# Performance work log

Hardware: AMD Instinct MI355X
Metric: run time of the kernel (lower is better)

Reference implementation:

```python
import jax, jax.numpy as jnp
import numpy as np
from jax import lax

B, T, V, LAT, U, P = 256, 128, 42, 200, 512, 3  # batch, seq, vocab, latent, lstm units, num_prop


def setup_inputs() -> dict:
    key = jax.random.key(0)
    ks = jax.random.split(key, 40)
    g = lambda i, shape, s=0.05: (jax.random.normal(ks[i], shape, jnp.float32) * s)
    inp = {
        'X': jax.random.randint(ks[0], (B, T), 0, V, jnp.int64 if jax.config.jax_enable_x64 else jnp.int32),
        'Y': jax.random.randint(ks[1], (B, T), 0, V, jnp.int32),
        'C': jax.random.normal(ks[2], (B, P), jnp.float32),
        'L': jax.random.randint(ks[3], (B,), 1, T + 1, jnp.int32),
        'eps': jax.random.normal(ks[4], (B, LAT), jnp.float32),
        'emb_enc': g(5, (V, LAT), 0.1),
        'emb_dec': g(6, (V, LAT), 0.1),
        # encoder stacked LSTM: layer0 input dim = LAT + P, layers 1-2 input dim = U
        'enc_k0': g(7, (LAT + P, 4 * U)), 'enc_rk0': g(8, (U, 4 * U)), 'enc_b0': jnp.zeros((4 * U,), jnp.float32),
        'enc_k1': g(9, (U, 4 * U)), 'enc_rk1': g(10, (U, 4 * U)), 'enc_b1': jnp.zeros((4 * U,), jnp.float32),
        'enc_k2': g(11, (U, 4 * U)), 'enc_rk2': g(12, (U, 4 * U)), 'enc_b2': jnp.zeros((4 * U,), jnp.float32),
        # decoder stacked LSTM: layer0 input dim = 2*LAT + P
        'dec_k0': g(13, (2 * LAT + P, 4 * U)), 'dec_rk0': g(14, (U, 4 * U)), 'dec_b0': jnp.zeros((4 * U,), jnp.float32),
        'dec_k1': g(15, (U, 4 * U)), 'dec_rk1': g(16, (U, 4 * U)), 'dec_b1': jnp.zeros((4 * U,), jnp.float32),
        'dec_k2': g(17, (U, 4 * U)), 'dec_rk2': g(18, (U, 4 * U)), 'dec_b2': jnp.zeros((4 * U,), jnp.float32),
        'Wm': g(19, (U, LAT)), 'bm': jnp.zeros((LAT,), jnp.float32),
        'Ws': g(20, (U, LAT)), 'bs': jnp.zeros((LAT,), jnp.float32),
        'Wo': g(21, (U, V)), 'bo': jnp.zeros((V,), jnp.float32),
    }
    return inp


def _lstm_step(x, h, c, k, rk, b):
    # Keras LSTMCell gate order: i, f, g(candidate), o
    z = x @ k + h @ rk + b
    i, f, gg, o = jnp.split(z, 4, axis=-1)
    c2 = jax.nn.sigmoid(f) * c + jax.nn.sigmoid(i) * jnp.tanh(gg)
    h2 = jax.nn.sigmoid(o) * jnp.tanh(c2)
    return h2, c2


def _run_stacked(inp, params):
    # inp: [B, T, D]; params: list of 3 (kernel, recurrent_kernel, bias)
    b = inp.shape[0]
    init = tuple((jnp.zeros((b, U), inp.dtype), jnp.zeros((b, U), inp.dtype)) for _ in range(3))

    def scan_fn(carry, x_t):
        h_in = x_t
        new = []
        for (h, c), (k, rk, bb) in zip(carry, params):
            h2, c2 = _lstm_step(h_in, h, c, k, rk, bb)
            new.append((h2, c2))
            h_in = h2
        return tuple(new), h_in

    carry, ys = lax.scan(scan_fn, init, jnp.swapaxes(inp, 0, 1))
    return jnp.swapaxes(ys, 0, 1), carry  # [B,T,U], final states


def reference(X, Y, C, L, eps, emb_enc, emb_dec,
              enc_k0, enc_rk0, enc_b0, enc_k1, enc_rk1, enc_b1, enc_k2, enc_rk2, enc_b2,
              dec_k0, dec_rk0, dec_b0, dec_k1, dec_rk1, dec_b1, dec_k2, dec_rk2, dec_b2,
              Wm, bm, Ws, bs, Wo, bo):
    enc_params = [(enc_k0, enc_rk0, enc_b0), (enc_k1, enc_rk1, enc_b1), (enc_k2, enc_rk2, enc_b2)]
    dec_params = [(dec_k0, dec_rk0, dec_b0), (dec_k1, dec_rk1, dec_b1), (dec_k2, dec_rk2, dec_b2)]

    # ---- encode ----
    Xe = emb_enc[X]                                       # [B,T,LAT]
    Ct = jnp.broadcast_to(C[:, None, :], (B, T, P))
    enc_in = jnp.concatenate([Xe, Ct], axis=-1)           # [B,T,LAT+P]
    _, enc_states = _run_stacked(enc_in, enc_params)
    h = enc_states[-1][1]                                 # CELL state of last layer (state[-1][1])
    mean = h @ Wm + bm
    log_sigma = h @ Ws + bs
    z = mean + jnp.exp(log_sigma / 2.0) * eps             # [B,LAT]

    # ---- decode ----
    Zt = jnp.broadcast_to(z[:, None, :], (B, T, LAT))
    Xd = emb_dec[X]
    dec_in = jnp.concatenate([Zt, Xd, Ct], axis=-1)       # [B,T,2*LAT+P]
    dec_out, _ = _run_stacked(dec_in, dec_params)
    pre = dec_out @ Wo + bo                               # pre-softmax logits [B,T,V]

    # ---- losses ----
    logp = jax.nn.log_softmax(pre, axis=-1)
    ce = -jnp.take_along_axis(logp, Y[..., None].astype(jnp.int32), axis=-1)[..., 0]  # [B,T]
    weights = (jnp.arange(T)[None, :] < L[:, None]).astype(jnp.float32)
    recon = jnp.mean(ce * weights)
    latent = -0.5 * jnp.mean(1.0 + log_sigma - jnp.square(mean) - jnp.exp(log_sigma))
    loss = recon + latent
    return loss, recon, latent
```

## Files before the change

### kernel.cpp

```cpp
#include <hip/hip_runtime.h>

#define B_ 256
#define T_ 128
#define V_ 42
#define LAT_ 200
#define U_ 512
#define G4_ 2048
#define NBLK 196
#define FI(r, m) ((((r) * 2) + (m)) * 32)

typedef unsigned short ushort_t;
typedef __attribute__((ext_vector_type(8))) short bf8;
typedef __attribute__((ext_vector_type(4))) float f4;

__device__ __forceinline__ float bf2f(ushort_t u) {
  union { unsigned int i; float f; } v; v.i = ((unsigned int)u) << 16; return v.f;
}
__device__ __forceinline__ ushort_t f2bf(float f) {
  union { float f; unsigned int i; } v; v.f = f;
  unsigned int r = v.i + 0x7fffu + ((v.i >> 16) & 1u);
  return (ushort_t)(r >> 16);
}
__device__ __forceinline__ float sigf(float x) { return 1.f / (1.f + __expf(-x)); }
__device__ __forceinline__ float tanhfast(float x) {
  float e = __expf(2.f * x);
  return 1.f - 2.f / (e + 1.f);
}

__device__ __forceinline__ void st_wt_b16(void* p, ushort_t v) {
  unsigned int vv = v;
  asm volatile("global_store_short %0, %1, off sc0 sc1" :: "v"(p), "v"(vv) : "memory");
}
__device__ __forceinline__ void st_wt_b32(void* p, unsigned int v) {
  asm volatile("global_store_dword %0, %1, off sc0 sc1" :: "v"(p), "v"(v) : "memory");
}
__device__ __forceinline__ void wait_vm0() {
  asm volatile("s_waitcnt vmcnt(0)" ::: "memory");
}

__global__ __launch_bounds__(256) void table_kernel(const float* emb, const float* k0, int roff, float* table) {
  int v = blockIdx.x, tid = threadIdx.x;
  __shared__ float e[LAT_];
  for (int i = tid; i < LAT_; i += 256) e[i] = emb[v * LAT_ + i];
  __syncthreads();
  for (int j = tid; j < G4_; j += 256) {
    float s = 0.f;
    for (int n = 0; n < LAT_; n++) s += e[n] * k0[(size_t)(roff + n) * G4_ + j];
    table[v * G4_ + j] = s;
  }
}

__device__ __forceinline__ size_t mat_off_u4(int m) {
  if (m == 0) return 0;
  if (m == 1) return 147456;
  if (m < 10) return 360448 + (size_t)(m - 2) * 131072;
  return 1409024;
}

struct SwzSrc {
  const float *enc_rk0, *enc_k0, *enc_b0;
  const float *dec_rk0, *dec_k0, *dec_b0;
  const float *tabE, *tabD;
  const float *encK1, *encR1, *encK2, *encR2;
  const float *decK1, *decR1, *decK2, *decR2;
  const float *Wo;
  ushort_t* dst;
};

__device__ float swz_val(const SwzSrc& s, int mat, int k, int n) {
  switch (mat) {
    case 0: {
      if (k < 512) return s.enc_rk0[(size_t)k * G4_ + n];
      int i = k - 512;
      if (i < 42) return s.tabE[(size_t)i * G4_ + n];
      if (i < 45) return s.enc_k0[(size_t)(200 + i - 42) * G4_ + n];
      if (i == 45) return s.enc_b0[n];
      return 0.f;
    }
    case 1: {
      if (k < 512) return s.dec_rk0[(size_t)k * G4_ + n];
      int i = k - 512;
      if (i < 200) return s.dec_k0[(size_t)i * G4_ + n];
      if (i < 256) return 0.f;
      i -= 256;
      if (i < 42) return s.tabD[(size_t)i * G4_ + n];
      if (i < 45) return s.dec_k0[(size_t)(400 + i - 42) * G4_ + n];
      if (i == 45) return s.dec_b0[n];
      return 0.f;
    }
    case 2: return s.encK1[(size_t)k * G4_ + n];
    case 3: return s.encR1[(size_t)k * G4_ + n];
    case 4: return s.encK2[(size_t)k * G4_ + n];
    case 5: return s.encR2[(size_t)k * G4_ + n];
    case 6: return s.decK1[(size_t)k * G4_ + n];
    case 7: return s.decR1[(size_t)k * G4_ + n];
    case 8: return s.decK2[(size_t)k * G4_ + n];
    case 9: return s.decR2[(size_t)k * G4_ + n];
    default: return (n < V_) ? s.Wo[(size_t)k * V_ + n] : 0.f;
  }
}

__global__ __launch_bounds__(256) void swz_ext_kernel(SwzSrc s) {
  int b = blockIdx.x, tid = threadIdx.x;
  int mat, nt16;
  if (b < 1280) { mat = b >> 7; nt16 = b & 127; } else { mat = 10; nt16 = b - 1280; }
  int ktMax = (mat == 0) ? 18 : (mat == 1) ? 26 : 16;
  int lane = tid & 63, l15 = lane & 15, q = lane >> 4;
  int n = nt16 * 16 + l15;
  uint4* dst = (uint4*)s.dst;
  size_t off = mat_off_u4(mat);
  for (int kt = tid >> 6; kt < ktMax; kt += 4) {
    ushort_t o[8];
    int kb = kt * 32 + q * 8;
#pragma unroll
    for (int j = 0; j < 8; j++) o[j] = f2bf(swz_val(s, mat, kb + j, n));
    dst[off + ((size_t)nt16 * ktMax + kt) * 64 + lane] = *(const uint4*)o;
  }
}

struct PP {
  const ushort_t* swz;
  ushort_t *he0a, *he0b, *he1a, *he1b, *he2a, *he2b;
  ushort_t *hd0a, *hd0b, *hd1a, *hd1b, *hd2a, *hd2b;
  float* c2g; ushort_t* zf16; float* sums; int* bar; int* gen; int* flg; float* out;
  const float *enc_b1, *enc_b2, *dec_b1, *dec_b2;
  const float *Wm, *bm, *Ws, *bs, *eps, *C, *bo;
  const int *X, *Y, *Lb;
};

__device__ __forceinline__ void grid_barrier(int* bar, int* gen) {
  __builtin_amdgcn_fence(__ATOMIC_RELEASE, "agent");
  __syncthreads();
  if (threadIdx.x == 0) {
    int g = __hip_atomic_load(gen, __ATOMIC_RELAXED, __HIP_MEMORY_SCOPE_AGENT);
    if (__hip_atomic_fetch_add(bar, 1, __ATOMIC_ACQ_REL, __HIP_MEMORY_SCOPE_AGENT) == NBLK - 1) {
      __hip_atomic_store(bar, 0, __ATOMIC_RELAXED, __HIP_MEMORY_SCOPE_AGENT);
      __hip_atomic_store(gen, g + 1, __ATOMIC_RELEASE, __HIP_MEMORY_SCOPE_AGENT);
    } else {
      int gg;
      do {
        __builtin_amdgcn_s_sleep(1);
        gg = __hip_atomic_load(gen, __ATOMIC_ACQUIRE, __HIP_MEMORY_SCOPE_AGENT);
      } while (gg == g);
    }
  }
  __syncthreads();
  __builtin_amdgcn_fence(__ATOMIC_ACQUIRE, "agent");
}

__device__ __forceinline__ void wait_flags(const int* f, int cnt, int target) {
  int lane = threadIdx.x & 63;
  const int* a = f + (lane < cnt ? lane : 0);
  bool bad;
  do {
    int v = __hip_atomic_load(a, __ATOMIC_RELAXED, __HIP_MEMORY_SCOPE_AGENT);
    bad = (lane < cnt) && (v < target);
  } while (__ballot(bad) != 0ull);
}

#define MFMA(a, bfrag, c) __builtin_amdgcn_mfma_f32_16x16x32_bf16((a), (bfrag), (c), 0, 0, 0)

__global__ __launch_bounds__(256, 1) void persist(PP p) {
  __shared__ uint4 wlds4[8192];
  const int b = blockIdx.x, tid = threadIdx.x;
  const int lane = tid & 63, w = tid >> 6, q = lane >> 4, l15 = lane & 15;
  const int role = b < 64 ? 0 : b < 128 ? 1 : b < 192 ? 2 : 3;
  const int idx = b & 63;
  const int ut = idx >> 1, m0 = (idx & 1) * 128;
  const int mi = idx & 1;
  const int rw = m0 + w * 32;
  const int u = ut * 16 + l15;
  const uint4* swzU4 = (const uint4*)p.swz;
  const int cb = b - 192;

  unsigned char* tok = (unsigned char*)wlds4 + 106496;
  unsigned char* ytok = (unsigned char*)wlds4 + 49152;

  ushort_t* hE[3][2] = {{p.he0a, p.he0b}, {p.he1a, p.he1b}, {p.he2a, p.he2b}};
  ushort_t* hD[3][2] = {{p.hd0a, p.hd0b}, {p.hd1a, p.hd1b}, {p.hd2a, p.hd2b}};

  ushort_t cb0[2][3];
  if (role == 0) {
#pragma unroll
    for (int ms = 0; ms < 2; ms++)
#pragma unroll
      for (int j = 0; j < 3; j++) cb0[ms][j] = f2bf(p.C[(rw + ms * 16 + l15) * 3 + j]);
  }

  const int pubidx = (role < 3) ? (FI(role, mi) + ut) : (FI(3, cb >> 1) + (cb & 1));

  float ce_local = 0.f;
  float boR0 = 0.f, boR1 = 0.f, boR2 = 0.f;
  int Lr[4] = {0, 0, 0, 0};
  int pub = 0;

  for (int phase = 0; phase < 2; phase++) {
    const bool dec = (phase == 1);
    ushort_t* (*hb)[2] = dec ? hD : hE;

    if (dec) {
      grid_barrier(p.bar, p.gen);
      if (b < 50) {
        int lat0 = b * 4;
        int row = tid;
        float m[4], ls[4];
#pragma unroll
        for (int lc = 0; lc < 4; lc++) { m[lc] = p.bm[lat0 + lc]; ls[lc] = p.bs[lat0 + lc]; }
        const float* cr = p.c2g + (size_t)row * U_;
        for (int k = 0; k < U_; k++) {
          float hv = cr[k];
#pragma unroll
          for (int lc = 0; lc < 4; lc++) {
            m[lc] += hv * p.Wm[k * LAT_ + lat0 + lc];
            ls[lc] += hv * p.Ws[k * LAT_ + lat0 + lc];
          }
        }
        float kl = 0.f;
#pragma unroll
        for (int lc = 0; lc < 4; lc++) {
          int lat = lat0 + lc;
          float zz = m[lc] + __expf(0.5f * ls[lc]) * p.eps[row * LAT_ + lat];
          p.zf16[row * 256 + lat] = f2bf(zz);
          kl += 1.f + ls[lc] - m[lc] * m[lc] - __expf(ls[lc]);
        }
        float* red = (float*)wlds4;
        red[tid] = kl; __syncthreads();
        for (int st = 128; st > 0; st >>= 1) { if (tid < st) red[tid] += red[tid + st]; __syncthreads(); }
        if (tid == 0) atomicAdd(p.sums + 1, red[0]);
      }
      __syncthreads();
    }

    const int KT = dec ? 26 : 18;
    if (role == 0) {
      int mat = dec ? 1 : 0;
      size_t mo = mat_off_u4(mat);
      for (int g = 0; g < 4; g++) {
        int nt16 = g * 32 + ut;
        size_t src = mo + (size_t)nt16 * KT * 64;
        int dst = g * KT * 64;
        for (int i = tid; i < KT * 64; i += 256) wlds4[dst + i] = swzU4[src + i];
      }
      if (!dec) {
        for (int i = tid; i < 128 * T_; i += 256) {
          int r = i >> 7, t = i & 127;
          tok[r * 133 + t] = (unsigned char)p.X[(size_t)(m0 + r) * T_ + t];
        }
      }
    } else if (role <= 2) {
      int matK = dec ? (role == 1 ? 6 : 8) : (role == 1 ? 2 : 4);
      for (int gm = 0; gm < 2; gm++) {
        size_t mo = mat_off_u4(matK + gm);
        for (int g = 0; g < 4; g++) {
          int nt16 = g * 32 + ut;
          size_t src = mo + (size_t)nt16 * 1024;
          int dst = gm * 4096 + g * 1024;
          for (int i = tid; i < 1024; i += 256) wlds4[dst + i] = swzU4[src + i];
        }
      }
    } else if (dec) {
      size_t mo = mat_off_u4(10);
      for (int i = tid; i < 3072; i += 256) wlds4[i] = swzU4[mo + i];
      for (int i = tid; i < 64 * T_; i += 256) {
        int r = i >> 7, t = i & 127;
        ytok[r * 133 + t] = (unsigned char)p.Y[(size_t)(cb * 64 + r) * T_ + t];
      }
      int r0c = cb * 64 + w * 16;
      boR0 = p.bo[l15]; boR1 = p.bo[16 + l15]; boR2 = (l15 < 10) ? p.bo[32 + l15] : 0.f;
#pragma unroll
      for (int r = 0; r < 4; r++) Lr[r] = p.Lb[r0c + q * 4 + r];
    }
    __syncthreads();

    float creg[2][4];
#pragma unroll
    for (int ms = 0; ms < 2; ms++)
#pragma unroll
      for (int r = 0; r < 4; r++) creg[ms][r] = 0.f;
    float bias[4] = {0.f, 0.f, 0.f, 0.f};
    if (role == 1 || role == 2) {
      const float* bb = dec ? (role == 1 ? p.dec_b1 : p.dec_b2) : (role == 1 ? p.enc_b1 : p.enc_b2);
#pragma unroll
      for (int g = 0; g < 4; g++) bias[g] = bb[g * 512 + u];
    }

    const int* myp = nullptr; int myc = 0;
    if (role == 0) {
      if (w == 0) { myp = p.flg + FI(0, mi); myc = 32; }
      else if (w == 1) { myp = p.flg + FI(1, mi); myc = 32; }
    } else if (role == 1) {
      if (w == 0) { myp = p.flg + FI(0, mi); myc = 32; }
      else if (w == 1) { myp = p.flg + FI(1, mi); myc = 32; }
      else if (w == 2) { myp = p.flg + FI(2, mi); myc = 32; }
    } else if (role == 2) {
      if (w == 0) { myp = p.flg + FI(1, mi); myc = 32; }
      else if (w == 1) { myp = p.flg + FI(2, mi); myc = 32; }
      else if (w == 2 && dec) { myp = p.flg + FI(3, mi); myc = 2; }
    } else {
      if (w == 0 && dec) { myp = p.flg + FI(2, cb >> 1); myc = 32; }
    }

    grid_barrier(p.bar, p.gen);

    bf8 zr0[8], zr1[8];
    if (role == 0 && dec) {
      const ushort_t* Az0 = p.zf16 + (rw + l15) * 256 + q * 8;
#pragma unroll
      for (int kz = 0; kz < 8; kz++) {
        zr0[kz] = *(const bf8*)(Az0 + kz * 32);
        zr1[kz] = *(const bf8*)(Az0 + 16 * 256 + kz * 32);
      }
    }

    const int smax = dec ? T_ + 3 : T_ + 2;
    for (int s = 0; s < smax; s++) {
      pub++;
      if (myc) wait_flags(myp, myc, pub - 1);
      __builtin_amdgcn_fence(__ATOMIC_ACQUIRE, "agent");
      __syncthreads();

      const int prv = (s & 1) ^ 1, cur = s & 1;
      const int lag = (role <= 2) ? role : 3;
      const int t = s - lag;
      if (t >= 0 && t < T_) {
        if (role == 3) {
          int r0c = cb * 64 + w * 16;
          const ushort_t* Ar = hb[2][prv] + (size_t)(r0c + l15) * U_ + q * 8;
          f4 a3[3];
#pragma unroll
          for (int nt = 0; nt < 3; nt++) a3[nt] = (f4){0.f, 0.f, 0.f, 0.f};
#pragma unroll 4
          for (int kt = 0; kt < 16; kt++) {
            bf8 a = *(const bf8*)(Ar + kt * 32);
#pragma unroll
            for (int nt = 0; nt < 3; nt++) {
              bf8 bbf = *(const bf8*)&wlds4[nt * 1024 + kt * 64 + lane];
              a3[nt] = MFMA(a, bbf, a3[nt]);
            }
          }
#pragma unroll
          for (int r = 0; r < 4; r++) {
            int row = r0c + q * 4 + r;
            float v0 = a3[0][r] + boR0;
            float v1 = a3[1][r] + boR1;
            float v2 = (l15 < 10) ? a3[2][r] + boR2 : -3.0e38f;
            float mx = fmaxf(fmaxf(v0, v1), v2);
            mx = fmaxf(mx, __shfl_xor(mx, 1)); mx = fmaxf(mx, __shfl_xor(mx, 2));
            mx = fmaxf(mx, __shfl_xor(mx, 4)); mx = fmaxf(mx, __shfl_xor(mx, 8));
            float se = __expf(v0 - mx) + __expf(v1 - mx) + ((l15 < 10) ? __expf(v2 - mx) : 0.f);
            int yv = ytok[(w * 16 + q * 4 + r) * 133 + t];
            float py = (l15 == yv ? v0 : 0.f) + (l15 + 16 == yv ? v1 : 0.f) + (l15 + 32 == yv ? v2 : 0.f);
            se += __shfl_xor(se, 1); se += __shfl_xor(se, 2); se += __shfl_xor(se, 4); se += __shfl_xor(se, 8);
            py += __shfl_xor(py, 1); py += __shfl_xor(py, 2); py += __shfl_xor(py, 4); py += __shfl_xor(py, 8);
            if (l15 == 0 && t < Lr[r]) ce_local += mx + __logf(se) - py;
          }
        } else {
          f4 acc[2][4];
#pragma unroll
          for (int ms = 0; ms < 2; ms++)
#pragma unroll
            for (int g = 0; g < 4; g++) acc[ms][g] = (f4){0.f, 0.f, 0.f, 0.f};

          const ushort_t* hin = hb[role][prv];
          ushort_t* hout = hb[role][cur];
          const ushort_t* Ah0 = hin + (size_t)(rw + l15) * U_ + q * 8;
          const ushort_t* Ah1 = Ah0 + 16 * U_;

          if (role == 0) {
            const int KT64 = KT * 64;
#pragma unroll 4
            for (int kt = 0; kt < 16; kt++) {
              bf8 a0 = *(const bf8*)(Ah0 + kt * 32);
              bf8 a1 = *(const bf8*)(Ah1 + kt * 32);
#pragma unroll
              for (int g = 0; g < 4; g++) {
                bf8 bbf = *(const bf8*)&wlds4[g * KT64 + kt * 64 + lane];
                acc[0][g] = MFMA(a0, bbf, acc[0][g]);
                acc[1][g] = MFMA(a1, bbf, acc[1][g]);
              }
            }
            if (dec) {
#pragma unroll
              for (int kz = 0; kz < 8; kz++) {
#pragma unroll
                for (int g = 0; g < 4; g++) {
                  bf8 bbf = *(const bf8*)&wlds4[g * KT64 + (16 + kz) * 64 + lane];
                  acc[0][g] = MFMA(zr0[kz], bbf, acc[0][g]);
                  acc[1][g] = MFMA(zr1[kz], bbf, acc[1][g]);
                }
              }
            }
            int xv0 = tok[(w * 32 + l15) * 133 + t];
            int xv1 = tok[(w * 32 + 16 + l15) * 133 + t];
#pragma unroll
            for (int ktc = 0; ktc < 2; ktc++) {
              union { ushort_t us[8]; bf8 v; } a0u, a1u;
#pragma unroll
              for (int j = 0; j < 8; j++) {
                int id = ktc * 32 + q * 8 + j;
                ushort_t v0 = (id == xv0) ? (ushort_t)0x3F80 : (ushort_t)0;
                ushort_t v1 = (id == xv1) ? (ushort_t)0x3F80 : (ushort_t)0;
                if (id >= 42 && id < 45) { v0 = cb0[0][id - 42]; v1 = cb0[1][id - 42]; }
                if (id == 45) { v0 = 0x3F80; v1 = 0x3F80; }
                a0u.us[j] = v0; a1u.us[j] = v1;
              }
              int kt = KT - 2 + ktc;
#pragma unroll
              for (int g = 0; g < 4; g++) {
                bf8 bbf = *(const bf8*)&wlds4[g * KT64 + kt * 64 + lane];
                acc[0][g] = MFMA(a0u.v, bbf, acc[0][g]);
                acc[1][g] = MFMA(a1u.v, bbf, acc[1][g]);
              }
            }
          } else {
            const ushort_t* xin = hb[role - 1][prv];
            const ushort_t* Ax0 = xin + (size_t)(rw + l15) * U_ + q * 8;
            const ushort_t* Ax1 = Ax0 + 16 * U_;
#pragma unroll 4
            for (int kt = 0; kt < 16; kt++) {
              bf8 a0 = *(const bf8*)(Ax0 + kt * 32);
              bf8 a1 = *(const bf8*)(Ax1 + kt * 32);
#pragma unroll
              for (int g = 0; g < 4; g++) {
                bf8 bbf = *(const bf8*)&wlds4[g * 1024 + kt * 64 + lane];
                acc[0][g] = MFMA(a0, bbf, acc[0][g]);
                acc[1][g] = MFMA(a1, bbf, acc[1][g]);
              }
            }
#pragma unroll 4
            for (int kt = 0; kt < 16; kt++) {
              bf8 a0 = *(const bf8*)(Ah0 + kt * 32);
              bf8 a1 = *(const bf8*)(Ah1 + kt * 32);
#pragma unroll
              for (int g = 0; g < 4; g++) {
                bf8 bbf = *(const bf8*)&wlds4[4096 + g * 1024 + kt * 64 + lane];
                acc[0][g] = MFMA(a0, bbf, acc[0][g]);
                acc[1][g] = MFMA(a1, bbf, acc[1][g]);
              }
            }
          }

#pragma unroll
          for (int ms = 0; ms < 2; ms++)
#pragma unroll
            for (int r = 0; r < 4; r++) {
              int row = rw + ms * 16 + q * 4 + r;
              float zi = acc[ms][0][r] + bias[0];
              float zf = acc[ms][1][r] + bias[1];
              float zg = acc[ms][2][r] + bias[2];
              float zo = acc[ms][3][r] + bias[3];
              float cp = creg[ms][r];
              float cn = sigf(zf) * cp + sigf(zi) * tanhfast(zg);
              float hn = sigf(zo) * tanhfast(cn);
              creg[ms][r] = cn;
              st_wt_b16(&hout[(size_t)row * U_ + u], f2bf(hn));
              if (!dec && role == 2 && t == T_ - 1) p.c2g[(size_t)row * U_ + u] = cn;
            }
        }
      }
      wait_vm0();
      __syncthreads();
      if (tid == 0) st_wt_b32(p.flg + pubidx, (unsigned int)pub);
    }
  }

  if (role == 3 && l15 == 0) atomicAdd(p.sums + 0, ce_local);
  grid_barrier(p.bar, p.gen);
  if (b == 0 && tid == 0) {
    float recon = p.sums[0] * (1.f / ((float)B_ * (float)T_));
    float latent = -0.5f * p.sums[1] * (1.f / ((float)B_ * (float)LAT_));
    p.out[0] = recon + latent;
    p.out[1] = recon;
    p.out[2] = latent;
  }
}

extern "C" void kernel_launch(void* const* d_in, const int* in_sizes, int n_in,
                              void* d_out, int out_size, void* d_ws, size_t ws_size,
                              hipStream_t stream) {
  const int*   X       = (const int*)d_in[0];
  const int*   Y       = (const int*)d_in[1];
  const float* C       = (const float*)d_in[2];
  const int*   L       = (const int*)d_in[3];
  const float* eps     = (const float*)d_in[4];
  const float* emb_enc = (const float*)d_in[5];
  const float* emb_dec = (const float*)d_in[6];
  const float* enc_k0  = (const float*)d_in[7];
  const float* enc_rk0 = (const float*)d_in[8];
  const float* enc_b0  = (const float*)d_in[9];
  const float* enc_k1  = (const float*)d_in[10];
  const float* enc_rk1 = (const float*)d_in[11];
  const float* enc_b1  = (const float*)d_in[12];
  const float* enc_k2  = (const float*)d_in[13];
  const float* enc_rk2 = (const float*)d_in[14];
  const float* enc_b2  = (const float*)d_in[15];
  const float* dec_k0  = (const float*)d_in[16];
  const float* dec_rk0 = (const float*)d_in[17];
  const float* dec_b0  = (const float*)d_in[18];
  const float* dec_k1  = (const float*)d_in[19];
  const float* dec_rk1 = (const float*)d_in[20];
  const float* dec_b1  = (const float*)d_in[21];
  const float* dec_k2  = (const float*)d_in[22];
  const float* dec_rk2 = (const float*)d_in[23];
  const float* dec_b2  = (const float*)d_in[24];
  const float* Wm      = (const float*)d_in[25];
  const float* bm      = (const float*)d_in[26];
  const float* Ws      = (const float*)d_in[27];
  const float* bs      = (const float*)d_in[28];
  const float* Wo      = (const float*)d_in[29];
  const float* bo      = (const float*)d_in[30];
  float* out = (float*)d_out;
  (void)in_sizes; (void)n_in; (void)out_size; (void)ws_size;

  char* wsb = (char*)d_ws;
  size_t o = 0;
  auto take = [&](size_t bytes) -> char* { char* p = wsb + o; o += (bytes + 255) & ~(size_t)255; return p; };

  ushort_t* hE[3][2]; ushort_t* hD[3][2];
  for (int l = 0; l < 3; l++) for (int pi = 0; pi < 2; pi++) hE[l][pi] = (ushort_t*)take((size_t)B_ * U_ * 2);
  for (int l = 0; l < 3; l++) for (int pi = 0; pi < 2; pi++) hD[l][pi] = (ushort_t*)take((size_t)B_ * U_ * 2);
  float* c2g  = (float*)take((size_t)B_ * U_ * 4);
  ushort_t* zf16 = (ushort_t*)take((size_t)B_ * 256 * 2);
  float* sums = (float*)take(8);
  int* bar = (int*)take(4);
  int* gen = (int*)take(4);
  int* flg = (int*)take(4 * 2 * 32 * 4);
  size_t zero_bytes = o;
  ushort_t* swz = (ushort_t*)take((size_t)1412096 * 16);
  float* tabE = (float*)take((size_t)V_ * G4_ * 4);
  float* tabD = (float*)take((size_t)V_ * G4_ * 4);

  hipMemsetAsync(wsb, 0, zero_bytes, stream);
  table_kernel<<<V_, 256, 0, stream>>>(emb_enc, enc_k0, 0, tabE);
  table_kernel<<<V_, 256, 0, stream>>>(emb_dec, dec_k0, 200, tabD);

  SwzSrc ss;
  ss.enc_rk0 = enc_rk0; ss.enc_k0 = enc_k0; ss.enc_b0 = enc_b0;
  ss.dec_rk0 = dec_rk0; ss.dec_k0 = dec_k0; ss.dec_b0 = dec_b0;
  ss.tabE = tabE; ss.tabD = tabD;
  ss.encK1 = enc_k1; ss.encR1 = enc_rk1; ss.encK2 = enc_k2; ss.encR2 = enc_rk2;
  ss.decK1 = dec_k1; ss.decR1 = dec_rk1; ss.decK2 = dec_k2; ss.decR2 = dec_rk2;
  ss.Wo = Wo; ss.dst = swz;
  swz_ext_kernel<<<1283, 256, 0, stream>>>(ss);

  PP pp;
  pp.swz = swz;
  pp.he0a = hE[0][0]; pp.he0b = hE[0][1]; pp.he1a = hE[1][0]; pp.he1b = hE[1][1];
  pp.he2a = hE[2][0]; pp.he2b = hE[2][1];
  pp.hd0a = hD[0][0]; pp.hd0b = hD[0][1]; pp.hd1a = hD[1][0]; pp.hd1b = hD[1][1];
  pp.hd2a = hD[2][0]; pp.hd2b = hD[2][1];
  pp.c2g = c2g; pp.zf16 = zf16; pp.sums = sums; pp.bar = bar; pp.gen = gen; pp.flg = flg; pp.out = out;
  pp.enc_b1 = enc_b1; pp.enc_b2 = enc_b2; pp.dec_b1 = dec_b1; pp.dec_b2 = dec_b2;
  pp.Wm = Wm; pp.bm = bm; pp.Ws = Ws; pp.bs = bs; pp.eps = eps; pp.C = C; pp.bo = bo;
  pp.X = X; pp.Y = Y; pp.Lb = L;
  persist<<<NBLK, 256, 0, stream>>>(pp);
}
```

Baseline: 5.500 ms.

## Use per-timestep hidden-state ring buffers to drop write-after-read flag waits

Replaces the double-buffered per-layer hidden-state arrays with a ring that keeps one slot per timestep for each layer, shared by encoder and decoder. Because a slot is never overwritten while a consumer might still read it, blocks no longer wait on their downstream layer's flags. The output-projection blocks stop publishing flags and skip encoder-phase work. The flag spin loop gains a sleep and the acquire fence after waiting is removed. In exchange the workspace grows to about 100 MB of hidden-state storage, reads touch fresh memory each step instead of a hot buffer, and dropping the fence relies on the write-through stores being visible without it.

```diff
diff --git a/kernel.cpp b/kernel.cpp
--- a/kernel.cpp
+++ b/kernel.cpp
@@ -8,14 +8,13 @@
 #define G4_ 2048
 #define NBLK 196
 #define FI(r, m) ((((r) * 2) + (m)) * 32)
+#define SLOT_ ((size_t)B_ * U_)
+#define LS_ ((size_t)129 * SLOT_)
 
 typedef unsigned short ushort_t;
 typedef __attribute__((ext_vector_type(8))) short bf8;
 typedef __attribute__((ext_vector_type(4))) float f4;
 
-__device__ __forceinline__ float bf2f(ushort_t u) {
-  union { unsigned int i; float f; } v; v.i = ((unsigned int)u) << 16; return v.f;
-}
 __device__ __forceinline__ ushort_t f2bf(float f) {
   union { float f; unsigned int i; } v; v.f = f;
   unsigned int r = v.i + 0x7fffu + ((v.i >> 16) & 1u);
@@ -120,8 +119,7 @@
 
 struct PP {
   const ushort_t* swz;
-  ushort_t *he0a, *he0b, *he1a, *he1b, *he2a, *he2b;
-  ushort_t *hd0a, *hd0b, *hd1a, *hd1b, *hd2a, *hd2b;
+  ushort_t* ring;
   float* c2g; ushort_t* zf16; float* sums; int* bar; int* gen; int* flg; float* out;
   const float *enc_b1, *enc_b2, *dec_b1, *dec_b2;
   const float *Wm, *bm, *Ws, *bs, *eps, *C, *bo;
@@ -155,7 +153,9 @@
   do {
     int v = __hip_atomic_load(a, __ATOMIC_RELAXED, __HIP_MEMORY_SCOPE_AGENT);
     bad = (lane < cnt) && (v < target);
-  } while (__ballot(bad) != 0ull);
+    if (__ballot(bad) == 0ull) break;
+    __builtin_amdgcn_s_sleep(1);
+  } while (true);
 }
 
 #define MFMA(a, bfrag, c) __builtin_amdgcn_mfma_f32_16x16x32_bf16((a), (bfrag), (c), 0, 0, 0)
@@ -166,8 +166,9 @@
   const int lane = tid & 63, w = tid >> 6, q = lane >> 4, l15 = lane & 15;
   const int role = b < 64 ? 0 : b < 128 ? 1 : b < 192 ? 2 : 3;
   const int idx = b & 63;
-  const int ut = idx >> 1, m0 = (idx & 1) * 128;
+  const int ut = idx >> 1;
   const int mi = idx & 1;
+  const int m0 = mi * 128;
   const int rw = m0 + w * 32;
   const int u = ut * 16 + l15;
   const uint4* swzU4 = (const uint4*)p.swz;
@@ -176,9 +177,6 @@
   unsigned char* tok = (unsigned char*)wlds4 + 106496;
   unsigned char* ytok = (unsigned char*)wlds4 + 49152;
 
-  ushort_t* hE[3][2] = {{p.he0a, p.he0b}, {p.he1a, p.he1b}, {p.he2a, p.he2b}};
-  ushort_t* hD[3][2] = {{p.hd0a, p.hd0b}, {p.hd1a, p.hd1b}, {p.hd2a, p.hd2b}};
-
   ushort_t cb0[2][3];
   if (role == 0) {
 #pragma unroll
@@ -187,7 +185,7 @@
       for (int j = 0; j < 3; j++) cb0[ms][j] = f2bf(p.C[(rw + ms * 16 + l15) * 3 + j]);
   }
 
-  const int pubidx = (role < 3) ? (FI(role, mi) + ut) : (FI(3, cb >> 1) + (cb & 1));
+  const int pubidx = FI(role, mi) + ut;
 
   float ce_local = 0.f;
   float boR0 = 0.f, boR1 = 0.f, boR2 = 0.f;
@@ -196,7 +194,6 @@
 
   for (int phase = 0; phase < 2; phase++) {
     const bool dec = (phase == 1);
-    ushort_t* (*hb)[2] = dec ? hD : hE;
 
     if (dec) {
       grid_barrier(p.bar, p.gen);
@@ -287,15 +284,12 @@
     const int* myp = nullptr; int myc = 0;
     if (role == 0) {
       if (w == 0) { myp = p.flg + FI(0, mi); myc = 32; }
-      else if (w == 1) { myp = p.flg + FI(1, mi); myc = 32; }
     } else if (role == 1) {
       if (w == 0) { myp = p.flg + FI(0, mi); myc = 32; }
       else if (w == 1) { myp = p.flg + FI(1, mi); myc = 32; }
-      else if (w == 2) { myp = p.flg + FI(2, mi); myc = 32; }
     } else if (role == 2) {
       if (w == 0) { myp = p.flg + FI(1, mi); myc = 32; }
       else if (w == 1) { myp = p.flg + FI(2, mi); myc = 32; }
-      else if (w == 2 && dec) { myp = p.flg + FI(3, mi); myc = 2; }
     } else {
       if (w == 0 && dec) { myp = p.flg + FI(2, cb >> 1); myc = 32; }
     }
@@ -316,16 +310,14 @@
     for (int s = 0; s < smax; s++) {
       pub++;
       if (myc) wait_flags(myp, myc, pub - 1);
-      __builtin_amdgcn_fence(__ATOMIC_ACQUIRE, "agent");
       __syncthreads();
 
-      const int prv = (s & 1) ^ 1, cur = s & 1;
       const int lag = (role <= 2) ? role : 3;
       const int t = s - lag;
-      if (t >= 0 && t < T_) {
-        if (role == 3) {
+      if (role == 3) {
+        if (dec && t >= 0 && t < T_) {
           int r0c = cb * 64 + w * 16;
-          const ushort_t* Ar = hb[2][prv] + (size_t)(r0c + l15) * U_ + q * 8;
+          const ushort_t* Ar = p.ring + 2 * LS_ + (size_t)(t + 1) * SLOT_ + (size_t)(r0c + l15) * U_ + q * 8;
           f4 a3[3];
 #pragma unroll
           for (int nt = 0; nt < 3; nt++) a3[nt] = (f4){0.f, 0.f, 0.f, 0.f};
@@ -340,7 +332,6 @@
           }
 #pragma unroll
           for (int r = 0; r < 4; r++) {
-            int row = r0c + q * 4 + r;
             float v0 = a3[0][r] + boR0;
             float v1 = a3[1][r] + boR1;
             float v2 = (l15 < 10) ? a3[2][r] + boR2 : -3.0e38f;
@@ -354,113 +345,113 @@
             py += __shfl_xor(py, 1); py += __shfl_xor(py, 2); py += __shfl_xor(py, 4); py += __shfl_xor(py, 8);
             if (l15 == 0 && t < Lr[r]) ce_local += mx + __logf(se) - py;
           }
+        }
+      } else if (t >= 0 && t < T_) {
+        f4 acc[2][4];
+#pragma unroll
+        for (int ms = 0; ms < 2; ms++)
+#pragma unroll
+          for (int g = 0; g < 4; g++) acc[ms][g] = (f4){0.f, 0.f, 0.f, 0.f};
+
+        const ushort_t* hin = p.ring + (size_t)role * LS_ + (size_t)t * SLOT_;
+        ushort_t* hout = p.ring + (size_t)role * LS_ + (size_t)(t + 1) * SLOT_;
+        const ushort_t* Ah0 = hin + (size_t)(rw + l15) * U_ + q * 8;
+        const ushort_t* Ah1 = Ah0 + 16 * U_;
+
+        if (role == 0) {
+          const int KT64 = KT * 64;
+#pragma unroll 4
+          for (int kt = 0; kt < 16; kt++) {
+            bf8 a0 = *(const bf8*)(Ah0 + kt * 32);
+            bf8 a1 = *(const bf8*)(Ah1 + kt * 32);
+#pragma unroll
+            for (int g = 0; g < 4; g++) {
+              bf8 bbf = *(const bf8*)&wlds4[g * KT64 + kt * 64 + lane];
+              acc[0][g] = MFMA(a0, bbf, acc[0][g]);
+              acc[1][g] = MFMA(a1, bbf, acc[1][g]);
+            }
+          }
+          if (dec) {
+#pragma unroll
+            for (int kz = 0; kz < 8; kz++) {
+#pragma unroll
+              for (int g = 0; g < 4; g++) {
+                bf8 bbf = *(const bf8*)&wlds4[g * KT64 + (16 + kz) * 64 + lane];
+                acc[0][g] = MFMA(zr0[kz], bbf, acc[0][g]);
+                acc[1][g] = MFMA(zr1[kz], bbf, acc[1][g]);
+              }
+            }
+          }
+          int xv0 = tok[(w * 32 + l15) * 133 + t];
+          int xv1 = tok[(w * 32 + 16 + l15) * 133 + t];
+#pragma unroll
+          for (int ktc = 0; ktc < 2; ktc++) {
+            union { ushort_t us[8]; bf8 v; } a0u, a1u;
+#pragma unroll
+            for (int j = 0; j < 8; j++) {
+              int id = ktc * 32 + q * 8 + j;
+              ushort_t v0 = (id == xv0) ? (ushort_t)0x3F80 : (ushort_t)0;
+              ushort_t v1 = (id == xv1) ? (ushort_t)0x3F80 : (ushort_t)0;
+              if (id >= 42 && id < 45) { v0 = cb0[0][id - 42]; v1 = cb0[1][id - 42]; }
+              if (id == 45) { v0 = 0x3F80; v1 = 0x3F80; }
+              a0u.us[j] = v0; a1u.us[j] = v1;
+            }
+            int kt = KT - 2 + ktc;
+#pragma unroll
+            for (int g = 0; g < 4; g++) {
+              bf8 bbf = *(const bf8*)&wlds4[g * KT64 + kt * 64 + lane];
+              acc[0][g] = MFMA(a0u.v, bbf, acc[0][g]);
+              acc[1][g] = MFMA(a1u.v, bbf, acc[1][g]);
+            }
+          }
         } else {
-          f4 acc[2][4];
-#pragma unroll
-          for (int ms = 0; ms < 2; ms++)
-#pragma unroll
-            for (int g = 0; g < 4; g++) acc[ms][g] = (f4){0.f, 0.f, 0.f, 0.f};
-
-          const ushort_t* hin = hb[role][prv];
-          ushort_t* hout = hb[role][cur];
-          const ushort_t* Ah0 = hin + (size_t)(rw + l15) * U_ + q * 8;
-          const ushort_t* Ah1 = Ah0 + 16 * U_;
-
-          if (role == 0) {
-            const int KT64 = KT * 64;
+          const ushort_t* xin = p.ring + (size_t)(role - 1) * LS_ + (size_t)(t + 1) * SLOT_;
+          const ushort_t* Ax0 = xin + (size_t)(rw + l15) * U_ + q * 8;
+          const ushort_t* Ax1 = Ax0 + 16 * U_;
 #pragma unroll 4
-            for (int kt = 0; kt < 16; kt++) {
-              bf8 a0 = *(const bf8*)(Ah0 + kt * 32);
-              bf8 a1 = *(const bf8*)(Ah1 + kt * 32);
-#pragma unroll
-              for (int g = 0; g < 4; g++) {
-                bf8 bbf = *(const bf8*)&wlds4[g * KT64 + kt * 64 + lane];
-                acc[0][g] = MFMA(a0, bbf, acc[0][g]);
-                acc[1][g] = MFMA(a1, bbf, acc[1][g]);
-              }
-            }
-            if (dec) {
-#pragma unroll
-              for (int kz = 0; kz < 8; kz++) {
-#pragma unroll
-                for (int g = 0; g < 4; g++) {
-                  bf8 bbf = *(const bf8*)&wlds4[g * KT64 + (16 + kz) * 64 + lane];
-                  acc[0][g] = MFMA(zr0[kz], bbf, acc[0][g]);
-                  acc[1][g] = MFMA(zr1[kz], bbf, acc[1][g]);
-                }
-              }
-            }
-            int xv0 = tok[(w * 32 + l15) * 133 + t];
-            int xv1 = tok[(w * 32 + 16 + l15) * 133 + t];
-#pragma unroll
-            for (int ktc = 0; ktc < 2; ktc++) {
-              union { ushort_t us[8]; bf8 v; } a0u, a1u;
-#pragma unroll
-              for (int j = 0; j < 8; j++) {
-                int id = ktc * 32 + q * 8 + j;
-                ushort_t v0 = (id == xv0) ? (ushort_t)0x3F80 : (ushort_t)0;
-                ushort_t v1 = (id == xv1) ? (ushort_t)0x3F80 : (ushort_t)0;
-                if (id >= 42 && id < 45) { v0 = cb0[0][id - 42]; v1 = cb0[1][id - 42]; }
-                if (id == 45) { v0 = 0x3F80; v1 = 0x3F80; }
-                a0u.us[j] = v0; a1u.us[j] = v1;
-              }
-              int kt = KT - 2 + ktc;
-#pragma unroll
-              for (int g = 0; g < 4; g++) {
-                bf8 bbf = *(const bf8*)&wlds4[g * KT64 + kt * 64 + lane];
-                acc[0][g] = MFMA(a0u.v, bbf, acc[0][g]);
-                acc[1][g] = MFMA(a1u.v, bbf, acc[1][g]);
-              }
-            }
-          } else {
-            const ushort_t* xin = hb[role - 1][prv];
-            const ushort_t* Ax0 = xin + (size_t)(rw + l15) * U_ + q * 8;
-            const ushort_t* Ax1 = Ax0 + 16 * U_;
+          for (int kt = 0; kt < 16; kt++) {
+            bf8 a0 = *(const bf8*)(Ax0 + kt * 32);
+            bf8 a1 = *(const bf8*)(Ax1 + kt * 32);
+#pragma unroll
+            for (int g = 0; g < 4; g++) {
+              bf8 bbf = *(const bf8*)&wlds4[g * 1024 + kt * 64 + lane];
+              acc[0][g] = MFMA(a0, bbf, acc[0][g]);
+              acc[1][g] = MFMA(a1, bbf, acc[1][g]);
+            }
+          }
 #pragma unroll 4
-            for (int kt = 0; kt < 16; kt++) {
-              bf8 a0 = *(const bf8*)(Ax0 + kt * 32);
-              bf8 a1 = *(const bf8*)(Ax1 + kt * 32);
-#pragma unroll
-              for (int g = 0; g < 4; g++) {
-                bf8 bbf = *(const bf8*)&wlds4[g * 1024 + kt * 64 + lane];
-                acc[0][g] = MFMA(a0, bbf, acc[0][g]);
-                acc[1][g] = MFMA(a1, bbf, acc[1][g]);
-              }
-            }
-#pragma unroll 4
-            for (int kt = 0; kt < 16; kt++) {
-              bf8 a0 = *(const bf8*)(Ah0 + kt * 32);
-              bf8 a1 = *(const bf8*)(Ah1 + kt * 32);
-#pragma unroll
-              for (int g = 0; g < 4; g++) {
-                bf8 bbf = *(const bf8*)&wlds4[4096 + g * 1024 + kt * 64 + lane];
-                acc[0][g] = MFMA(a0, bbf, acc[0][g]);
-                acc[1][g] = MFMA(a1, bbf, acc[1][g]);
-              }
-            }
-          }
-
-#pragma unroll
-          for (int ms = 0; ms < 2; ms++)
-#pragma unroll
-            for (int r = 0; r < 4; r++) {
-              int row = rw + ms * 16 + q * 4 + r;
-              float zi = acc[ms][0][r] + bias[0];
-              float zf = acc[ms][1][r] + bias[1];
-              float zg = acc[ms][2][r] + bias[2];
-              float zo = acc[ms][3][r] + bias[3];
-              float cp = creg[ms][r];
-              float cn = sigf(zf) * cp + sigf(zi) * tanhfast(zg);
-              float hn = sigf(zo) * tanhfast(cn);
-              creg[ms][r] = cn;
-              st_wt_b16(&hout[(size_t)row * U_ + u], f2bf(hn));
-              if (!dec && role == 2 && t == T_ - 1) p.c2g[(size_t)row * U_ + u] = cn;
-            }
+          for (int kt = 0; kt < 16; kt++) {
+            bf8 a0 = *(const bf8*)(Ah0 + kt * 32);
+            bf8 a1 = *(const bf8*)(Ah1 + kt * 32);
+#pragma unroll
+            for (int g = 0; g < 4; g++) {
+              bf8 bbf = *(const bf8*)&wlds4[4096 + g * 1024 + kt * 64 + lane];
+              acc[0][g] = MFMA(a0, bbf, acc[0][g]);
+              acc[1][g] = MFMA(a1, bbf, acc[1][g]);
+            }
+          }
         }
+
+#pragma unroll
+        for (int ms = 0; ms < 2; ms++)
+#pragma unroll
+          for (int r = 0; r < 4; r++) {
+            int row = rw + ms * 16 + q * 4 + r;
+            float zi = acc[ms][0][r] + bias[0];
+            float zf = acc[ms][1][r] + bias[1];
+            float zg = acc[ms][2][r] + bias[2];
+            float zo = acc[ms][3][r] + bias[3];
+            float cp = creg[ms][r];
+            float cn = sigf(zf) * cp + sigf(zi) * tanhfast(zg);
+            float hn = sigf(zo) * tanhfast(cn);
+            creg[ms][r] = cn;
+            st_wt_b16(&hout[(size_t)row * U_ + u], f2bf(hn));
+            if (!dec && role == 2 && t == T_ - 1) p.c2g[(size_t)row * U_ + u] = cn;
+          }
       }
       wait_vm0();
       __syncthreads();
-      if (tid == 0) st_wt_b32(p.flg + pubidx, (unsigned int)pub);
+      if (tid == 0 && role < 3) st_wt_b32(p.flg + pubidx, (unsigned int)pub);
     }
   }
 
@@ -516,9 +507,6 @@
   size_t o = 0;
   auto take = [&](size_t bytes) -> char* { char* p = wsb + o; o += (bytes + 255) & ~(size_t)255; return p; };
 
-  ushort_t* hE[3][2]; ushort_t* hD[3][2];
-  for (int l = 0; l < 3; l++) for (int pi = 0; pi < 2; pi++) hE[l][pi] = (ushort_t*)take((size_t)B_ * U_ * 2);
-  for (int l = 0; l < 3; l++) for (int pi = 0; pi < 2; pi++) hD[l][pi] = (ushort_t*)take((size_t)B_ * U_ * 2);
   float* c2g  = (float*)take((size_t)B_ * U_ * 4);
   ushort_t* zf16 = (ushort_t*)take((size_t)B_ * 256 * 2);
   float* sums = (float*)take(8);
@@ -526,11 +514,15 @@
   int* gen = (int*)take(4);
   int* flg = (int*)take(4 * 2 * 32 * 4);
   size_t zero_bytes = o;
+  ushort_t* ring = (ushort_t*)take(3 * LS_ * 2);
   ushort_t* swz = (ushort_t*)take((size_t)1412096 * 16);
   float* tabE = (float*)take((size_t)V_ * G4_ * 4);
   float* tabD = (float*)take((size_t)V_ * G4_ * 4);
 
   hipMemsetAsync(wsb, 0, zero_bytes, stream);
+  for (int l = 0; l < 3; l++)
+    hipMemsetAsync(ring + (size_t)l * LS_, 0, SLOT_ * 2, stream);
+
   table_kernel<<<V_, 256, 0, stream>>>(emb_enc, enc_k0, 0, tabE);
   table_kernel<<<V_, 256, 0, stream>>>(emb_dec, dec_k0, 200, tabD);
 
@@ -544,11 +536,7 @@
   swz_ext_kernel<<<1283, 256, 0, stream>>>(ss);
 
   PP pp;
-  pp.swz = swz;
-  pp.he0a = hE[0][0]; pp.he0b = hE[0][1]; pp.he1a = hE[1][0]; pp.he1b = hE[1][1];
-  pp.he2a = hE[2][0]; pp.he2b = hE[2][1];
-  pp.hd0a = hD[0][0]; pp.hd0b = hD[0][1]; pp.hd1a = hD[1][0]; pp.hd1b = hD[1][1];
-  pp.hd2a = hD[2][0]; pp.hd2b = hD[2][1];
+  pp.swz = swz; pp.ring = ring;
   pp.c2g = c2g; pp.zf16 = zf16; pp.sums = sums; pp.bar = bar; pp.gen = gen; pp.flg = flg; pp.out = out;
   pp.enc_b1 = enc_b1; pp.enc_b2 = enc_b2; pp.dec_b1 = dec_b1; pp.dec_b2 = dec_b2;
   pp.Wm = Wm; pp.bm = bm; pp.Ws = Ws; pp.bs = bs; pp.eps = eps; pp.C = C; pp.bo = bo;
```

New measurement: 5.007 ms. 1.1x faster.
